# Kernel tuning notes

Hardware: AMD Instinct MI355X
Metric: run time of the kernel (lower is better)

## Reference

```python
import jax, jax.numpy as jnp
import numpy as np

# PFNLayer constants from init_kwargs
X_VOXEL = 0.16
Y_VOXEL = 0.16
X_OFFSET = 0.16 / 2 + 0.0        # voxel_size[0]/2 + point_cloud_range[0]
# NOTE: original code (bug) uses x_offset for the y branch too; replicated.

P_TOTAL = 200000
MAX_PTS = 32
C_IN = 4


def setup_inputs() -> dict:
    key = jax.random.key(0)
    k1, k2, k3 = jax.random.split(key, 3)
    pillars = jax.random.normal(k1, (P_TOTAL, MAX_PTS, C_IN), dtype=jnp.float32)
    coors_batch = jax.random.randint(k2, (P_TOTAL, 4), 0, 400, dtype=jnp.int32)
    # at least 1 valid point per pillar (voxelizer never emits empty pillars)
    npoints_per_pillar = jax.random.randint(k3, (P_TOTAL,), 1, MAX_PTS + 1, dtype=jnp.int32)
    return {"pillars": pillars, "coors_batch": coors_batch,
            "npoints_per_pillar": npoints_per_pillar}


def reference(pillars, coors_batch, npoints_per_pillar):
    # pillars: (P, N, 4); coors_batch: (P, 4) int; npoints_per_pillar: (P,) int
    n = npoints_per_pillar.astype(pillars.dtype)  # (P,)
    # arithmetic mean of xyz over the pillar (sum over padded slots / true count)
    points_mean = jnp.sum(pillars[:, :, :3], axis=1, keepdims=True) / n[:, None, None]
    center_off = pillars[:, :, :3] - points_mean                      # (P, N, 3)
    cx = coors_batch[:, None, 1:2].astype(pillars.dtype) * X_VOXEL + X_OFFSET
    cy = coors_batch[:, None, 2:3].astype(pillars.dtype) * Y_VOXEL + X_OFFSET  # bug: x_offset
    off_x = pillars[:, :, :1] - cx                                    # (P, N, 1)
    off_y = pillars[:, :, 1:2] - cy                                   # (P, N, 1)
    # torch code: concat then overwrite channels 0,1 with off_x, off_y
    features = jnp.concatenate(
        [off_x, off_y, pillars[:, :, 2:], center_off, off_x, off_y], axis=-1)  # (P, N, 9)
    # zero out padded point slots
    mask = (jnp.arange(MAX_PTS, dtype=jnp.int32)[None, :] < npoints_per_pillar[:, None])
    features = features * mask[:, :, None].astype(features.dtype)
    features = jnp.transpose(features, (0, 2, 1))                     # (P, 9, N)
    return coors_batch, features
```

## Files before the change

kernel.cpp:

```cpp
#include <hip/hip_runtime.h>


#define X_VOXEL 0.16f
#define Y_VOXEL 0.16f
#define X_OFFSET 0.08f
#define MAX_PTS 32

__global__ __launch_bounds__(256) void pfn_kernel(
    const float4* __restrict__ pillars,
    const int*    __restrict__ coors,
    const int*    __restrict__ npoints,
    float*        __restrict__ out_coors,
    float*        __restrict__ out_feat,
    int P)
{
    int tid    = blockIdx.x * blockDim.x + threadIdx.x;
    int pillar = tid >> 5;
    int lane   = tid & 31;
    if (pillar >= P) return;

    float4 pt = pillars[(size_t)pillar * MAX_PTS + lane];

    float sx = pt.x, sy = pt.y, sz = pt.z;
    #pragma unroll
    for (int off = 16; off > 0; off >>= 1) {
        sx += __shfl_xor(sx, off, 32);
        sy += __shfl_xor(sy, off, 32);
        sz += __shfl_xor(sz, off, 32);
    }

    int np = npoints[pillar];
    float n  = (float)np;
    float mx = sx / n, my = sy / n, mz = sz / n;

    int cv = coors[pillar * 4 + (lane & 3)];
    float cx = (float)__shfl(cv, 1, 32) * X_VOXEL + X_OFFSET;
    float cy = (float)__shfl(cv, 2, 32) * Y_VOXEL + X_OFFSET;

    float m  = (lane < np) ? 1.0f : 0.0f;

    float f0 = (pt.x - cx) * m;
    float f1 = (pt.y - cy) * m;

    float* o = out_feat + (size_t)pillar * 9 * MAX_PTS;
    o[  0 + lane] = f0;
    o[ 32 + lane] = f1;
    o[ 64 + lane] = pt.z * m;
    o[ 96 + lane] = pt.w * m;
    o[128 + lane] = (pt.x - mx) * m;
    o[160 + lane] = (pt.y - my) * m;
    o[192 + lane] = (pt.z - mz) * m;
    o[224 + lane] = f0;
    o[256 + lane] = f1;

    if (lane < 4) out_coors[pillar * 4 + lane] = (float)cv;
}

extern "C" void kernel_launch(void* const* d_in, const int* in_sizes, int n_in,
                              void* d_out, int out_size, void* d_ws, size_t ws_size,
                              hipStream_t stream) {
    const float* pillars = (const float*)d_in[0];
    const int*   coors   = (const int*)d_in[1];
    const int*   npoints = (const int*)d_in[2];
    int P = in_sizes[2];

    float* out       = (float*)d_out;
    float* out_coors = out;
    float* out_feat  = out + (size_t)P * 4;

    const int threads = 256;
    const int ppb = threads / 32;
    int grid = (P + ppb - 1) / ppb;
    pfn_kernel<<<grid, threads, 0, stream>>>(
        (const float4*)pillars, coors, npoints, out_coors, out_feat, P);
}
```

Baseline: 309.3 us.

## Process four points per thread with float4 loads and vectorized stores

```diff
diff --git a/kernel.cpp b/kernel.cpp
--- a/kernel.cpp
+++ b/kernel.cpp
@@ -14,46 +14,67 @@
     float*        __restrict__ out_feat,
     int P)
 {
-    int tid    = blockIdx.x * blockDim.x + threadIdx.x;
-    int pillar = tid >> 5;
-    int lane   = tid & 31;
-    if (pillar >= P) return;
+    int tid = blockIdx.x * blockDim.x + threadIdx.x;
+    int p   = tid >> 3;
+    int g   = tid & 7;
 
-    float4 pt = pillars[(size_t)pillar * MAX_PTS + lane];
-
-    float sx = pt.x, sy = pt.y, sz = pt.z;
-    #pragma unroll
-    for (int off = 16; off > 0; off >>= 1) {
-        sx += __shfl_xor(sx, off, 32);
-        sy += __shfl_xor(sy, off, 32);
-        sz += __shfl_xor(sz, off, 32);
+    int cbase = blockIdx.x * 32;
+    if (threadIdx.x < 32 && cbase + threadIdx.x < P) {
+        int4 c4 = ((const int4*)coors)[cbase + threadIdx.x];
+        ((float4*)out_coors)[cbase + threadIdx.x] =
+            make_float4((float)c4.x, (float)c4.y, (float)c4.z, (float)c4.w);
     }
 
-    int np = npoints[pillar];
+    if (p >= P) return;
+
+    const float4* src = pillars + (size_t)p * MAX_PTS + 4 * g;
+    float4 pt0 = src[0], pt1 = src[1], pt2 = src[2], pt3 = src[3];
+
+    float sx = pt0.x + pt1.x + pt2.x + pt3.x;
+    float sy = pt0.y + pt1.y + pt2.y + pt3.y;
+    float sz = pt0.z + pt1.z + pt2.z + pt3.z;
+    #pragma unroll
+    for (int off = 4; off > 0; off >>= 1) {
+        sx += __shfl_xor(sx, off, 8);
+        sy += __shfl_xor(sy, off, 8);
+        sz += __shfl_xor(sz, off, 8);
+    }
+
+    int np = npoints[p];
     float n  = (float)np;
     float mx = sx / n, my = sy / n, mz = sz / n;
 
-    int cv = coors[pillar * 4 + (lane & 3)];
-    float cx = (float)__shfl(cv, 1, 32) * X_VOXEL + X_OFFSET;
-    float cy = (float)__shfl(cv, 2, 32) * Y_VOXEL + X_OFFSET;
+    int cv = coors[p * 4 + (g & 3)];
+    float cx = (float)__shfl(cv, 1, 8) * X_VOXEL + X_OFFSET;
+    float cy = (float)__shfl(cv, 2, 8) * Y_VOXEL + X_OFFSET;
 
-    float m  = (lane < np) ? 1.0f : 0.0f;
+    float m0 = (4 * g + 0 < np) ? 1.0f : 0.0f;
+    float m1 = (4 * g + 1 < np) ? 1.0f : 0.0f;
+    float m2 = (4 * g + 2 < np) ? 1.0f : 0.0f;
+    float m3 = (4 * g + 3 < np) ? 1.0f : 0.0f;
 
-    float f0 = (pt.x - cx) * m;
-    float f1 = (pt.y - cy) * m;
+    float* o = out_feat + (size_t)p * 288 + 4 * g;
+    #define ST(c, e) ((float4*)(o + (c) * 32))[0] = make_float4( \
+        (pt0.e) * m0, (pt1.e) * m1, (pt2.e) * m2, (pt3.e) * m3)
 
-    float* o = out_feat + (size_t)pillar * 9 * MAX_PTS;
-    o[  0 + lane] = f0;
-    o[ 32 + lane] = f1;
-    o[ 64 + lane] = pt.z * m;
-    o[ 96 + lane] = pt.w * m;
-    o[128 + lane] = (pt.x - mx) * m;
-    o[160 + lane] = (pt.y - my) * m;
-    o[192 + lane] = (pt.z - mz) * m;
-    o[224 + lane] = f0;
-    o[256 + lane] = f1;
+    float4 ox = make_float4(pt0.x - cx, pt1.x - cx, pt2.x - cx, pt3.x - cx);
+    float4 oy = make_float4(pt0.y - cy, pt1.y - cy, pt2.y - cy, pt3.y - cy);
+    ox.x *= m0; ox.y *= m1; ox.z *= m2; ox.w *= m3;
+    oy.x *= m0; oy.y *= m1; oy.z *= m2; oy.w *= m3;
 
-    if (lane < 4) out_coors[pillar * 4 + lane] = (float)cv;
+    ((float4*)(o +   0))[0] = ox;
+    ((float4*)(o +  32))[0] = oy;
+    ST(2, z);
+    ST(3, w);
+    ((float4*)(o + 128))[0] = make_float4((pt0.x - mx) * m0, (pt1.x - mx) * m1,
+                                          (pt2.x - mx) * m2, (pt3.x - mx) * m3);
+    ((float4*)(o + 160))[0] = make_float4((pt0.y - my) * m0, (pt1.y - my) * m1,
+                                          (pt2.y - my) * m2, (pt3.y - my) * m3);
+    ((float4*)(o + 192))[0] = make_float4((pt0.z - mz) * m0, (pt1.z - mz) * m1,
+                                          (pt2.z - mz) * m2, (pt3.z - mz) * m3);
+    ((float4*)(o + 224))[0] = ox;
+    ((float4*)(o + 256))[0] = oy;
+    #undef ST
 }
 
 extern "C" void kernel_launch(void* const* d_in, const int* in_sizes, int n_in,
@@ -69,8 +90,8 @@
     float* out_feat  = out + (size_t)P * 4;
 
     const int threads = 256;
-    const int ppb = threads / 32;
-    int grid = (P + ppb - 1) / ppb;
+    long long total = (long long)P * 8;
+    int grid = (int)((total + threads - 1) / threads);
     pfn_kernel<<<grid, threads, 0, stream>>>(
         (const float4*)pillars, coors, npoints, out_coors, out_feat, P);
 }
```

Result: no change. 309.0 us (-0.1%).
